# Kernel optimization log

Hardware: AMD Instinct MI355X
Metric: run time of the kernel (lower is better)

Reference implementation:

```python
import jax, jax.numpy as jnp
import numpy as np

N = 100000
E = 1600000
D_IN = 128
HID = 128
OUT = 64


def _sage_conv(x, edge_index, W_l, W_r, b, num_nodes):
    # PyG SAGEConv (aggr='mean'): out = lin_l(mean_{j in N(i)} x_j) + lin_r(x_i)
    src, dst = edge_index[0], edge_index[1]
    msgs = x[src]  # [E, d] gather from source nodes
    summed = jax.ops.segment_sum(msgs, dst, num_segments=num_nodes)  # [N, d]
    cnt = jax.ops.segment_sum(jnp.ones((msgs.shape[0],), x.dtype), dst, num_segments=num_nodes)
    agg = summed / jnp.maximum(cnt, 1.0)[:, None]  # mean; isolated nodes -> 0
    return agg @ W_l + b + x @ W_r


def setup_inputs() -> dict:
    key = jax.random.key(0)
    ks = jax.random.split(key, 8)
    x = jax.random.normal(ks[0], (N, D_IN), dtype=jnp.float32)
    edge_index = jax.random.randint(ks[1], (2, E), 0, N, dtype=jnp.int64)
    s1 = 1.0 / np.sqrt(D_IN)
    s2 = 1.0 / np.sqrt(HID)
    W_l1 = jax.random.uniform(ks[2], (D_IN, HID), jnp.float32, -s1, s1)
    W_r1 = jax.random.uniform(ks[3], (D_IN, HID), jnp.float32, -s1, s1)
    b1 = jnp.zeros((HID,), jnp.float32)
    W_l2 = jax.random.uniform(ks[4], (HID, OUT), jnp.float32, -s2, s2)
    W_r2 = jax.random.uniform(ks[5], (HID, OUT), jnp.float32, -s2, s2)
    b2 = jnp.zeros((OUT,), jnp.float32)
    return {"x": x, "edge_index": edge_index, "W_l1": W_l1, "W_r1": W_r1,
            "b1": b1, "W_l2": W_l2, "W_r2": W_r2, "b2": b2}


def reference(x, edge_index, W_l1, W_r1, b1, W_l2, W_r2, b2):
    h = _sage_conv(x, edge_index, W_l1, W_r1, b1, N)
    h = jax.nn.relu(h)
    out = _sage_conv(h, edge_index, W_l2, W_r2, b2, N)
    return out
```

## Files before the change

kernel.cpp:

```cpp
#include <hip/hip_runtime.h>
#include <hip/hip_fp16.h>

typedef __attribute__((ext_vector_type(8))) short bf16x8;
typedef __attribute__((ext_vector_type(4))) float f32x4;

__device__ __forceinline__ f32x4 mfma16(bf16x8 a, bf16x8 b, f32x4 c) {
    return __builtin_amdgcn_mfma_f32_16x16x32_bf16(a, b, c, 0, 0, 0);
}

__device__ __forceinline__ unsigned short bf16_rte(float f) {
    unsigned int u = __float_as_uint(f);
    unsigned int r = (u + 0x7FFFu + ((u >> 16) & 1u)) >> 16;
    return (unsigned short)r;
}
__device__ __forceinline__ float bf16_f(unsigned short h) {
    return __uint_as_float(((unsigned int)h) << 16);
}

__device__ __forceinline__ void split8h(bf16x8 raw, bf16x8& hi, bf16x8& lo) {
#pragma unroll
    for (int j = 0; j < 8; ++j) {
        float f = __half2float(__ushort_as_half((unsigned short)raw[j]));
        unsigned short h = bf16_rte(f);
        hi[j] = (short)h;
        lo[j] = (short)bf16_rte(f - bf16_f(h));
    }
}

__device__ __forceinline__ void acc8(uint4 r, float4& A0, float4& A1) {
    float2 v0 = __half22float2(*(const __half2*)&r.x);
    float2 v1 = __half22float2(*(const __half2*)&r.y);
    float2 v2 = __half22float2(*(const __half2*)&r.z);
    float2 v3 = __half22float2(*(const __half2*)&r.w);
    A0.x += v0.x; A0.y += v0.y; A0.z += v1.x; A0.w += v1.y;
    A1.x += v2.x; A1.y += v2.y; A1.z += v3.x; A1.w += v3.y;
}

__device__ __forceinline__ void acc4(uint2 r, float4& A) {
    float2 v0 = __half22float2(*(const __half2*)&r.x);
    float2 v1 = __half22float2(*(const __half2*)&r.y);
    A.x += v0.x; A.y += v0.y; A.z += v1.x; A.w += v1.y;
}

#define MAXNB 1024

__global__ __launch_bounds__(256) void k_prep(
    const float* __restrict__ Wl1, const float* __restrict__ Wr1,
    const float* __restrict__ Wl2, const float* __restrict__ Wr2,
    unsigned short* __restrict__ w1ah, unsigned short* __restrict__ w1al,
    unsigned short* __restrict__ w1bh, unsigned short* __restrict__ w1bl,
    unsigned short* __restrict__ w2ah, unsigned short* __restrict__ w2al,
    unsigned short* __restrict__ w2bh, unsigned short* __restrict__ w2bl,
    const float* __restrict__ x, unsigned short* __restrict__ x16,
    const int* __restrict__ dst, int* __restrict__ bcnt,
    int E, int chunk, int xb, int nb, int total8) {
    __shared__ int hh[MAXNB];
    int b = blockIdx.x;
    int t = threadIdx.x;
    if (b < 192) {
        const float* W;
        unsigned short *hi, *lo;
        int F, e;
        if (b < 64)       { W = Wl1; hi = w1ah; lo = w1al; F = 128; e = b * 256 + t; }
        else if (b < 128) { W = Wr1; hi = w1bh; lo = w1bl; F = 128; e = (b - 64) * 256 + t; }
        else if (b < 160) { W = Wl2; hi = w2ah; lo = w2al; F = 64;  e = (b - 128) * 256 + t; }
        else              { W = Wr2; hi = w2bh; lo = w2bl; F = 64;  e = (b - 160) * 256 + t; }
        if (e >= 128 * F) return;
        int col = e >> 7, k = e & 127;
        float v = W[(size_t)k * F + col];
        unsigned short h = bf16_rte(v);
        hi[e] = h;
        lo[e] = bf16_rte(v - bf16_f(h));
    } else if (b < 192 + xb) {
        int i = (b - 192) * 256 + t;
        if (i >= total8) return;
        const float4* xp = (const float4*)x + (size_t)i * 2;
        float4 a = xp[0], bb = xp[1];
        bf16x8 o;
        o[0] = (short)__half_as_ushort(__float2half_rn(a.x));
        o[1] = (short)__half_as_ushort(__float2half_rn(a.y));
        o[2] = (short)__half_as_ushort(__float2half_rn(a.z));
        o[3] = (short)__half_as_ushort(__float2half_rn(a.w));
        o[4] = (short)__half_as_ushort(__float2half_rn(bb.x));
        o[5] = (short)__half_as_ushort(__float2half_rn(bb.y));
        o[6] = (short)__half_as_ushort(__float2half_rn(bb.z));
        o[7] = (short)__half_as_ushort(__float2half_rn(bb.w));
        *(bf16x8*)&x16[(size_t)i * 8] = o;
    } else {
        int cb = b - 192 - xb;
        for (int i = t; i < nb; i += 256) hh[i] = 0;
        __syncthreads();
        int base = cb * chunk;
        int end = min(base + chunk, E);
        for (int i = base + t; i < end; i += 256) atomicAdd(&hh[dst[i] >> 7], 1);
        __syncthreads();
        for (int i = t; i < nb; i += 256)
            if (hh[i]) atomicAdd(&bcnt[i], hh[i]);
    }
}


__global__ void k_bscan(const int* __restrict__ bcnt, int* __restrict__ boff,
                        int* __restrict__ bcur, int nb) {
    __shared__ int sh[1024];
    int t = threadIdx.x;
    int v = (t < nb) ? bcnt[t] : 0;
    sh[t] = v;
    __syncthreads();
    for (int off = 1; off < 1024; off <<= 1) {
        int u = (t >= off) ? sh[t - off] : 0;
        __syncthreads();
        sh[t] += u;
        __syncthreads();
    }
    if (t < nb) {
        int ex = sh[t] - v;
        boff[t] = ex;
        bcur[t] = ex;
    }
}

__global__ __launch_bounds__(256) void k_bscatter(
    const int* __restrict__ src, const int* __restrict__ dst,
    int* __restrict__ bcur, int2* __restrict__ pairs, int E, int chunk, int nb) {
    __shared__ int h[MAXNB];
    __shared__ int curs[MAXNB];
    int t = threadIdx.x;
    for (int i = t; i < nb; i += 256) h[i] = 0;
    __syncthreads();
    int base = blockIdx.x * chunk;
    int end = min(base + chunk, E);
    for (int i = base + t; i < end; i += 256) atomicAdd(&h[dst[i] >> 7], 1);
    __syncthreads();
    for (int i = t; i < nb; i += 256)
        curs[i] = h[i] ? atomicAdd(&bcur[i], h[i]) : 0;
    __syncthreads();
    for (int i = base + t; i < end; i += 256) {
        int d = dst[i];
        int p = atomicAdd(&curs[d >> 7], 1);
        pairs[p] = make_int2(d, src[i]);
    }
}

__global__ __launch_bounds__(256) void k_build(
    const int2* __restrict__ pairs, const int* __restrict__ boff,
    int* __restrict__ csr, int* __restrict__ start, int* __restrict__ deg,
    int n, int nb, int E) {
    __shared__ int scnt[128];
    __shared__ int soff[128];
    __shared__ int cur[128];
    int b = blockIdx.x;
    int t = threadIdx.x;
    int base = boff[b];
    int end = (b + 1 < nb) ? boff[b + 1] : E;
    if (t < 128) scnt[t] = 0;
    __syncthreads();
    for (int i = base + t; i < end; i += 256) {
        int2 e = pairs[i];
        atomicAdd(&scnt[e.x & 127], 1);
    }
    __syncthreads();
    if (t < 128) soff[t] = scnt[t];
    __syncthreads();
    for (int off = 1; off < 128; off <<= 1) {
        int val = 0;
        if (t < 128 && t >= off) val = soff[t - off];
        __syncthreads();
        if (t < 128) soff[t] += val;
        __syncthreads();
    }
    if (t < 128) {
        int c = scnt[t];
        int ex = soff[t] - c;
        int node = b * 128 + t;
        if (node < n) {
            start[node] = base + ex;
            deg[node] = c;
        }
        cur[t] = base + ex;
    }
    __syncthreads();
    for (int i = base + t; i < end; i += 256) {
        int2 e = pairs[i];
        int p = atomicAdd(&cur[e.x & 127], 1);
        csr[p] = e.y;
    }
}

#define SR 40

__global__ __launch_bounds__(256, 2) void fused1(
    const unsigned short* __restrict__ X,
    const int* __restrict__ csr, const int* __restrict__ start,
    const int* __restrict__ deg,
    const unsigned short* __restrict__ W0H, const unsigned short* __restrict__ W0L,
    const unsigned short* __restrict__ W1H, const unsigned short* __restrict__ W1L,
    const float* __restrict__ bias, unsigned short* __restrict__ dstH, int n) {
    constexpr int CT = 2;
    __shared__ unsigned short aHi[4][64 * SR], aLo[4][64 * SR];

    int t = threadIdx.x;
    int wv = t >> 6, l = t & 63, q = l >> 4, nl = l & 15;
    int wc = wv * 32;
    int node0 = blockIdx.x * 64;
    int sn = t >> 2, q4 = t & 3;
    int gn = min(node0 + sn, n - 1);

    {
        const unsigned short* p = X + (size_t)gn * 128 + q4 * 8;
        bf16x8 r[4];
#pragma unroll
        for (int c = 0; c < 4; ++c) r[c] = *(const bf16x8*)(p + c * 32);
        int base = sn * SR + q4 * 8;
#pragma unroll
        for (int c = 0; c < 4; ++c) {
            bf16x8 hi, lo;
            split8h(r[c], hi, lo);
            *(bf16x8*)&aHi[c][base] = hi;
            *(bf16x8*)&aLo[c][base] = lo;
        }
    }

    f32x4 acc[4][CT];
#pragma unroll
    for (int a = 0; a < 4; ++a)
#pragma unroll
        for (int b = 0; b < CT; ++b) acc[a][b] = (f32x4){0.f, 0.f, 0.f, 0.f};

    bf16x8 wh[2][CT], wl[2][CT];
#pragma unroll
    for (int uu = 0; uu < CT; ++uu) {
        int base = (wc + uu * 16 + nl) * 128 + q * 8;
        wh[0][uu] = *(const bf16x8*)&W0H[base];
        wl[0][uu] = *(const bf16x8*)&W0L[base];
    }
    __syncthreads();

#pragma unroll
    for (int c = 0; c < 4; ++c) {
        if (c < 3) {
#pragma unroll
            for (int uu = 0; uu < CT; ++uu) {
                int base = (wc + uu * 16 + nl) * 128 + (c + 1) * 32 + q * 8;
                wh[(c + 1) & 1][uu] = *(const bf16x8*)&W0H[base];
                wl[(c + 1) & 1][uu] = *(const bf16x8*)&W0L[base];
            }
        }
        bf16x8 ah[4], al[4];
#pragma unroll
        for (int tt = 0; tt < 4; ++tt) {
            int off = (tt * 16 + nl) * SR + q * 8;
            ah[tt] = *(const bf16x8*)&aHi[c][off];
            al[tt] = *(const bf16x8*)&aLo[c][off];
        }
        int cb = c & 1;
#pragma unroll
        for (int tt = 0; tt < 4; ++tt)
#pragma unroll
            for (int uu = 0; uu < CT; ++uu) {
                f32x4 a = acc[tt][uu];
                a = mfma16(al[tt], wh[cb][uu], a);
                a = mfma16(ah[tt], wl[cb][uu], a);
                a = mfma16(ah[tt], wh[cb][uu], a);
                acc[tt][uu] = a;
            }
    }
    __syncthreads();

    {
        int sub = l >> 4, fl = l & 15;
        int cch = fl >> 2, qq = fl & 3;
#pragma unroll 1
        for (int r4 = 0; r4 < 4; ++r4) {
            int nloc = wv * 16 + r4 * 4 + sub;
            int nc = min(node0 + nloc, n - 1);
            int s = start[nc], d = deg[nc];
            float4 A0 = {0.f, 0.f, 0.f, 0.f}, A1 = {0.f, 0.f, 0.f, 0.f};
            int j = 0;
            if (d >= 8) {
                int idx[8];
#pragma unroll
                for (int k = 0; k < 8; ++k) idx[k] = csr[s + k];
                for (; j + 16 <= d; j += 8) {
                    uint4 rr[8];
#pragma unroll
                    for (int k = 0; k < 8; ++k)
                        rr[k] = ((const uint4*)(X + (size_t)idx[k] * 128))[fl];
#pragma unroll
                    for (int k = 0; k < 8; ++k) idx[k] = csr[s + j + 8 + k];
#pragma unroll
                    for (int k = 0; k < 8; ++k) acc8(rr[k], A0, A1);
                }
                {
                    uint4 rr[8];
#pragma unroll
                    for (int k = 0; k < 8; ++k)
                        rr[k] = ((const uint4*)(X + (size_t)idx[k] * 128))[fl];
#pragma unroll
                    for (int k = 0; k < 8; ++k) acc8(rr[k], A0, A1);
                    j += 8;
                }
            }
            for (; j < d; ++j)
                acc8(((const uint4*)(X + (size_t)csr[s + j] * 128))[fl], A0, A1);
            float inv = 1.0f / (float)max(d, 1);
            float m[8] = {A0.x * inv, A0.y * inv, A0.z * inv, A0.w * inv,
                          A1.x * inv, A1.y * inv, A1.z * inv, A1.w * inv};
            bf16x8 hi, lo;
#pragma unroll
            for (int k = 0; k < 8; ++k) {
                unsigned short hh = bf16_rte(m[k]);
                hi[k] = (short)hh;
                lo[k] = (short)bf16_rte(m[k] - bf16_f(hh));
            }
            int base = nloc * SR + qq * 8;
            *(bf16x8*)&aHi[cch][base] = hi;
            *(bf16x8*)&aLo[cch][base] = lo;
        }
    }

#pragma unroll
    for (int uu = 0; uu < CT; ++uu) {
        int base = (wc + uu * 16 + nl) * 128 + q * 8;
        wh[0][uu] = *(const bf16x8*)&W1H[base];
        wl[0][uu] = *(const bf16x8*)&W1L[base];
    }
    __syncthreads();

#pragma unroll
    for (int c = 0; c < 4; ++c) {
        if (c < 3) {
#pragma unroll
            for (int uu = 0; uu < CT; ++uu) {
                int base = (wc + uu * 16 + nl) * 128 + (c + 1) * 32 + q * 8;
                wh[(c + 1) & 1][uu] = *(const bf16x8*)&W1H[base];
                wl[(c + 1) & 1][uu] = *(const bf16x8*)&W1L[base];
            }
        }
        bf16x8 ah[4], al[4];
#pragma unroll
        for (int tt = 0; tt < 4; ++tt) {
            int off = (tt * 16 + nl) * SR + q * 8;
            ah[tt] = *(const bf16x8*)&aHi[c][off];
            al[tt] = *(const bf16x8*)&aLo[c][off];
        }
        int cb = c & 1;
#pragma unroll
        for (int tt = 0; tt < 4; ++tt)
#pragma unroll
            for (int uu = 0; uu < CT; ++uu) {
                f32x4 a = acc[tt][uu];
                a = mfma16(al[tt], wh[cb][uu], a);
                a = mfma16(ah[tt], wl[cb][uu], a);
                a = mfma16(ah[tt], wh[cb][uu], a);
                acc[tt][uu] = a;
            }
    }
    __syncthreads();

    unsigned short* tb = &aHi[0][0];
#pragma unroll
    for (int uu = 0; uu < CT; ++uu) {
        int col = wc + uu * 16 + nl;
        float bv = bias[col];
#pragma unroll
        for (int tt = 0; tt < 4; ++tt)
#pragma unroll
            for (int r = 0; r < 4; ++r) {
                float vv = fmaxf(acc[tt][uu][r] + bv, 0.f);
                tb[(tt * 16 + q * 4 + r) * 136 + col] =
                    __half_as_ushort(__float2half_rn(vv));
            }
    }
    __syncthreads();
    int node = node0 + sn;
    if (node < n) {
        const unsigned short* sp = tb + sn * 136 + q4 * 32;
        unsigned short* dp = dstH + (size_t)node * 128 + q4 * 32;
#pragma unroll
        for (int i = 0; i < 4; ++i) *(bf16x8*)(dp + i * 8) = *(const bf16x8*)(sp + i * 8);
    }
}

__global__ __launch_bounds__(256, 2) void gemm2d(
    const unsigned short* __restrict__ H,
    const unsigned short* __restrict__ WaH, const unsigned short* __restrict__ WaL,
    const unsigned short* __restrict__ WbH, const unsigned short* __restrict__ WbL,
    const float* __restrict__ bias, unsigned short* __restrict__ p16,
    float* __restrict__ outF, int n) {
    constexpr int CT = 2;
    __shared__ unsigned short aHi[4][64 * SR], aLo[4][64 * SR];

    int t = threadIdx.x;
    int wv = t >> 6, l = t & 63, q = l >> 4, nl = l & 15;
    int ysel = wv >> 1;
    int wc = (wv & 1) * 32;
    int node0 = blockIdx.x * 64;
    int sn = t >> 2, q4 = t & 3;
    int gn = min(node0 + sn, n - 1);
    const unsigned short* WH = ysel ? WbH : WaH;
    const unsigned short* WL = ysel ? WbL : WaL;

    {
        const unsigned short* p = H + (size_t)gn * 128 + q4 * 8;
        bf16x8 r[4];
#pragma unroll
        for (int c = 0; c < 4; ++c) r[c] = *(const bf16x8*)(p + c * 32);
        int base = sn * SR + q4 * 8;
#pragma unroll
        for (int c = 0; c < 4; ++c) {
            bf16x8 hi, lo;
            split8h(r[c], hi, lo);
            *(bf16x8*)&aHi[c][base] = hi;
            *(bf16x8*)&aLo[c][base] = lo;
        }
    }

    f32x4 acc[4][CT];
#pragma unroll
    for (int a = 0; a < 4; ++a)
#pragma unroll
        for (int b = 0; b < CT; ++b) acc[a][b] = (f32x4){0.f, 0.f, 0.f, 0.f};

    bf16x8 wh[2][CT], wl[2][CT];
#pragma unroll
    for (int uu = 0; uu < CT; ++uu) {
        int base = (wc + uu * 16 + nl) * 128 + q * 8;
        wh[0][uu] = *(const bf16x8*)&WH[base];
        wl[0][uu] = *(const bf16x8*)&WL[base];
    }
    __syncthreads();

#pragma unroll
    for (int c = 0; c < 4; ++c) {
        if (c < 3) {
#pragma unroll
            for (int uu = 0; uu < CT; ++uu) {
                int base = (wc + uu * 16 + nl) * 128 + (c + 1) * 32 + q * 8;
                wh[(c + 1) & 1][uu] = *(const bf16x8*)&WH[base];
                wl[(c + 1) & 1][uu] = *(const bf16x8*)&WL[base];
            }
        }
        bf16x8 ah[4], al[4];
#pragma unroll
        for (int tt = 0; tt < 4; ++tt) {
            int off = (tt * 16 + nl) * SR + q * 8;
            ah[tt] = *(const bf16x8*)&aHi[c][off];
            al[tt] = *(const bf16x8*)&aLo[c][off];
        }
        int cb = c & 1;
#pragma unroll
        for (int tt = 0; tt < 4; ++tt)
#pragma unroll
            for (int uu = 0; uu < CT; ++uu) {
                f32x4 a = acc[tt][uu];
                a = mfma16(al[tt], wh[cb][uu], a);
                a = mfma16(ah[tt], wl[cb][uu], a);
                a = mfma16(ah[tt], wh[cb][uu], a);
                acc[tt][uu] = a;
            }
    }
    __syncthreads();

    unsigned short* tbu = &aHi[0][0];
    float* tbf = (float*)&aLo[0][0];
#pragma unroll
    for (int uu = 0; uu < CT; ++uu) {
        int col = wc + uu * 16 + nl;
        if (ysel) {
            float bv = bias[col];
#pragma unroll
            for (int tt = 0; tt < 4; ++tt)
#pragma unroll
                for (int r = 0; r < 4; ++r)
                    tbf[(tt * 16 + q * 4 + r) * 68 + col] = acc[tt][uu][r] + bv;
        } else {
#pragma unroll
            for (int tt = 0; tt < 4; ++tt)
#pragma unroll
                for (int r = 0; r < 4; ++r)
                    tbu[(tt * 16 + q * 4 + r) * 72 + col] =
                        __half_as_ushort(__float2half_rn(acc[tt][uu][r]));
        }
    }
    __syncthreads();
    int node = node0 + sn;
    if (node < n) {
        const unsigned short* spu = tbu + sn * 72 + q4 * 16;
        unsigned short* dpu = p16 + (size_t)node * 64 + q4 * 16;
        *(bf16x8*)dpu = *(const bf16x8*)spu;
        *(bf16x8*)(dpu + 8) = *(const bf16x8*)(spu + 8);
        const float* spf = tbf + sn * 68 + q4 * 16;
        float* dpf = outF + (size_t)node * 64 + q4 * 16;
#pragma unroll
        for (int i = 0; i < 4; ++i) *(float4*)(dpf + i * 4) = *(const float4*)(spf + i * 4);
    }
}

__global__ __launch_bounds__(256) void aggP(
    const unsigned short* __restrict__ tab, const int* __restrict__ csr,
    const int* __restrict__ start, const int* __restrict__ deg,
    float* __restrict__ outF, int n) {
    int gid = blockIdx.x * blockDim.x + threadIdx.x;
    int wave = gid >> 6, lane = gid & 63;
    int sub = lane >> 4, fl = lane & 15;
    int node = wave * 4 + sub;
    if (node >= n) return;
    int s = start[node], d = deg[node];
    float4 A = {0.f, 0.f, 0.f, 0.f};
    int j = 0;
    if (d >= 8) {
        int idx[8];
#pragma unroll
        for (int k = 0; k < 8; ++k) idx[k] = csr[s + k];
        for (; j + 16 <= d; j += 8) {
            uint2 rr[8];
#pragma unroll
            for (int k = 0; k < 8; ++k)
                rr[k] = ((const uint2*)(tab + (size_t)idx[k] * 64))[fl];
#pragma unroll
            for (int k = 0; k < 8; ++k) idx[k] = csr[s + j + 8 + k];
#pragma unroll
            for (int k = 0; k < 8; ++k) acc4(rr[k], A);
        }
        {
            uint2 rr[8];
#pragma unroll
            for (int k = 0; k < 8; ++k)
                rr[k] = ((const uint2*)(tab + (size_t)idx[k] * 64))[fl];
#pragma unroll
            for (int k = 0; k < 8; ++k) acc4(rr[k], A);
            j += 8;
        }
    }
    for (; j < d; ++j)
        acc4(((const uint2*)(tab + (size_t)csr[s + j] * 64))[fl], A);
    float inv = 1.0f / (float)max(d, 1);
    float* op = outF + (size_t)node * 64 + fl * 4;
    float4 cur = *(float4*)op;
    cur.x += A.x * inv;
    cur.y += A.y * inv;
    cur.z += A.z * inv;
    cur.w += A.w * inv;
    *(float4*)op = cur;
}


extern "C" void kernel_launch(void* const* d_in, const int* in_sizes, int n_in,
                              void* d_out, int out_size, void* d_ws, size_t ws_size,
                              hipStream_t stream) {
    const float* x   = (const float*)d_in[0];
    const int*   ei  = (const int*)d_in[1];
    const float* Wl1 = (const float*)d_in[2];
    const float* Wr1 = (const float*)d_in[3];
    const float* b1  = (const float*)d_in[4];
    const float* Wl2 = (const float*)d_in[5];
    const float* Wr2 = (const float*)d_in[6];
    const float* b2  = (const float*)d_in[7];
    float* out = (float*)d_out;

    int Nn = in_sizes[0] / 128;
    int E  = in_sizes[1] / 2;
    const int* src = ei;
    const int* dst = ei + E;
    int nb = (Nn + 127) / 128;

    char* ws = (char*)d_ws;
    auto alloc = [&](size_t bytes) -> char* {
        char* pp = ws;
        ws += (bytes + 255) / 256 * 256;
        return pp;
    };
    int* bcnt   = (int*)alloc((size_t)nb * 4);
    int* boff   = (int*)alloc((size_t)nb * 4);
    int* bcur   = (int*)alloc((size_t)nb * 4);
    int* start  = (int*)alloc((size_t)Nn * 4);
    int* deg    = (int*)alloc((size_t)Nn * 4);
    int* csr    = (int*)alloc((size_t)E * 4);
    unsigned short* x16  = (unsigned short*)alloc((size_t)Nn * 128 * 2);
    unsigned short* h16  = (unsigned short*)alloc((size_t)Nn * 128 * 2);
    unsigned short* p16  = (unsigned short*)alloc((size_t)Nn * 64 * 2);
    unsigned short* w1ah = (unsigned short*)alloc(128 * 128 * 2);
    unsigned short* w1al = (unsigned short*)alloc(128 * 128 * 2);
    unsigned short* w1bh = (unsigned short*)alloc(128 * 128 * 2);
    unsigned short* w1bl = (unsigned short*)alloc(128 * 128 * 2);
    unsigned short* w2ah = (unsigned short*)alloc(64 * 128 * 2);
    unsigned short* w2al = (unsigned short*)alloc(64 * 128 * 2);
    unsigned short* w2bh = (unsigned short*)alloc(64 * 128 * 2);
    unsigned short* w2bl = (unsigned short*)alloc(64 * 128 * 2);
    int2* pairs = (int2*)p16;

    hipMemsetAsync(bcnt, 0, (size_t)nb * 4, stream);

    int total8 = Nn * 16;
    int xb = (total8 + 255) / 256;
    int chunk = (E + 255) / 256;
    k_prep<<<192 + xb + 256, 256, 0, stream>>>(
        Wl1, Wr1, Wl2, Wr2,
        w1ah, w1al, w1bh, w1bl, w2ah, w2al, w2bh, w2bl,
        x, x16, dst, bcnt, E, chunk, xb, nb, total8);

    k_bscan<<<1, 1024, 0, stream>>>(bcnt, boff, bcur, nb);
    k_bscatter<<<256, 256, 0, stream>>>(src, dst, bcur, pairs, E, chunk, nb);
    k_build<<<nb, 256, 0, stream>>>(pairs, boff, csr, start, deg, Nn, nb, E);

    int gb = (Nn + 63) / 64;
    int ga = (Nn + 15) / 16;
    fused1<<<gb, 256, 0, stream>>>(x16, csr, start, deg,
                                   w1bh, w1bl, w1ah, w1al, b1, h16, Nn);
    gemm2d<<<gb, 256, 0, stream>>>(h16, w2ah, w2al, w2bh, w2bl, b2, p16, out, Nn);
    aggP<<<ga, 256, 0, stream>>>(p16, csr, start, deg, out, Nn);
}
```

Before: 336.1 us.

## Split layer-1 aggregation into standalone kernel and fuse both layer GEMMs

Measured after the change: 328.1 us. -2.4%, faster.

```diff
diff --git a/kernel.cpp b/kernel.cpp
--- a/kernel.cpp
+++ b/kernel.cpp
@@ -189,13 +189,65 @@
 
 #define SR 40
 
-__global__ __launch_bounds__(256, 2) void fused1(
-    const unsigned short* __restrict__ X,
-    const int* __restrict__ csr, const int* __restrict__ start,
-    const int* __restrict__ deg,
+__global__ __launch_bounds__(256) void aggF(
+    const unsigned short* __restrict__ tab, const int* __restrict__ csr,
+    const int* __restrict__ start, const int* __restrict__ deg,
+    unsigned short* __restrict__ outm, int n) {
+    int gid = blockIdx.x * blockDim.x + threadIdx.x;
+    int wave = gid >> 6, lane = gid & 63;
+    int sub = lane >> 4, fl = lane & 15;
+    int node = wave * 4 + sub;
+    if (node >= n) return;
+    int s = start[node], d = deg[node];
+    float4 A0 = {0.f, 0.f, 0.f, 0.f}, A1 = {0.f, 0.f, 0.f, 0.f};
+    int j = 0;
+    if (d >= 4) {
+        int i0 = csr[s], i1 = csr[s + 1], i2 = csr[s + 2], i3 = csr[s + 3];
+        for (; j + 8 <= d; j += 4) {
+            int n0 = csr[s + j + 4], n1 = csr[s + j + 5];
+            int n2 = csr[s + j + 6], n3 = csr[s + j + 7];
+            uint4 r0 = ((const uint4*)(tab + (size_t)i0 * 128))[fl];
+            uint4 r1 = ((const uint4*)(tab + (size_t)i1 * 128))[fl];
+            uint4 r2 = ((const uint4*)(tab + (size_t)i2 * 128))[fl];
+            uint4 r3 = ((const uint4*)(tab + (size_t)i3 * 128))[fl];
+            acc8(r0, A0, A1); acc8(r1, A0, A1);
+            acc8(r2, A0, A1); acc8(r3, A0, A1);
+            i0 = n0; i1 = n1; i2 = n2; i3 = n3;
+        }
+        {
+            uint4 r0 = ((const uint4*)(tab + (size_t)i0 * 128))[fl];
+            uint4 r1 = ((const uint4*)(tab + (size_t)i1 * 128))[fl];
+            uint4 r2 = ((const uint4*)(tab + (size_t)i2 * 128))[fl];
+            uint4 r3 = ((const uint4*)(tab + (size_t)i3 * 128))[fl];
+            acc8(r0, A0, A1); acc8(r1, A0, A1);
+            acc8(r2, A0, A1); acc8(r3, A0, A1);
+            j += 4;
+        }
+    }
+    for (; j < d; ++j)
+        acc8(((const uint4*)(tab + (size_t)csr[s + j] * 128))[fl], A0, A1);
+    float inv = 1.0f / (float)max(d, 1);
+    __half2 h0 = __floats2half2_rn(A0.x * inv, A0.y * inv);
+    __half2 h1 = __floats2half2_rn(A0.z * inv, A0.w * inv);
+    __half2 h2 = __floats2half2_rn(A1.x * inv, A1.y * inv);
+    __half2 h3 = __floats2half2_rn(A1.z * inv, A1.w * inv);
+    uint4 w;
+    w.x = *(unsigned int*)&h0;
+    w.y = *(unsigned int*)&h1;
+    w.z = *(unsigned int*)&h2;
+    w.w = *(unsigned int*)&h3;
+    *(uint4*)&outm[(size_t)node * 128 + fl * 8] = w;
+}
+
+__global__ __launch_bounds__(256, 2) void fused12(
+    const unsigned short* __restrict__ X, const unsigned short* __restrict__ XM,
     const unsigned short* __restrict__ W0H, const unsigned short* __restrict__ W0L,
     const unsigned short* __restrict__ W1H, const unsigned short* __restrict__ W1L,
-    const float* __restrict__ bias, unsigned short* __restrict__ dstH, int n) {
+    const float* __restrict__ b1,
+    const unsigned short* __restrict__ W2aH, const unsigned short* __restrict__ W2aL,
+    const unsigned short* __restrict__ W2bH, const unsigned short* __restrict__ W2bL,
+    const float* __restrict__ b2,
+    unsigned short* __restrict__ p16, float* __restrict__ outF, int n) {
     constexpr int CT = 2;
     __shared__ unsigned short aHi[4][64 * SR], aLo[4][64 * SR];
 
@@ -205,6 +257,20 @@
     int node0 = blockIdx.x * 64;
     int sn = t >> 2, q4 = t & 3;
     int gn = min(node0 + sn, n - 1);
+
+    bf16x8 s1r[4];
+    {
+        const unsigned short* p = XM + (size_t)gn * 128 + q4 * 8;
+#pragma unroll
+        for (int c = 0; c < 4; ++c) s1r[c] = *(const bf16x8*)(p + c * 32);
+    }
+    bf16x8 w1h0[CT], w1l0[CT];
+#pragma unroll
+    for (int uu = 0; uu < CT; ++uu) {
+        int base = (wc + uu * 16 + nl) * 128 + q * 8;
+        w1h0[uu] = *(const bf16x8*)&W1H[base];
+        w1l0[uu] = *(const bf16x8*)&W1L[base];
+    }
 
     {
         const unsigned short* p = X + (size_t)gn * 128 + q4 * 8;
@@ -268,63 +334,17 @@
     __syncthreads();
 
     {
-        int sub = l >> 4, fl = l & 15;
-        int cch = fl >> 2, qq = fl & 3;
-#pragma unroll 1
-        for (int r4 = 0; r4 < 4; ++r4) {
-            int nloc = wv * 16 + r4 * 4 + sub;
-            int nc = min(node0 + nloc, n - 1);
-            int s = start[nc], d = deg[nc];
-            float4 A0 = {0.f, 0.f, 0.f, 0.f}, A1 = {0.f, 0.f, 0.f, 0.f};
-            int j = 0;
-            if (d >= 8) {
-                int idx[8];
-#pragma unroll
-                for (int k = 0; k < 8; ++k) idx[k] = csr[s + k];
-                for (; j + 16 <= d; j += 8) {
-                    uint4 rr[8];
-#pragma unroll
-                    for (int k = 0; k < 8; ++k)
-                        rr[k] = ((const uint4*)(X + (size_t)idx[k] * 128))[fl];
-#pragma unroll
-                    for (int k = 0; k < 8; ++k) idx[k] = csr[s + j + 8 + k];
-#pragma unroll
-                    for (int k = 0; k < 8; ++k) acc8(rr[k], A0, A1);
-                }
-                {
-                    uint4 rr[8];
-#pragma unroll
-                    for (int k = 0; k < 8; ++k)
-                        rr[k] = ((const uint4*)(X + (size_t)idx[k] * 128))[fl];
-#pragma unroll
-                    for (int k = 0; k < 8; ++k) acc8(rr[k], A0, A1);
-                    j += 8;
-                }
-            }
-            for (; j < d; ++j)
-                acc8(((const uint4*)(X + (size_t)csr[s + j] * 128))[fl], A0, A1);
-            float inv = 1.0f / (float)max(d, 1);
-            float m[8] = {A0.x * inv, A0.y * inv, A0.z * inv, A0.w * inv,
-                          A1.x * inv, A1.y * inv, A1.z * inv, A1.w * inv};
+        int base = sn * SR + q4 * 8;
+#pragma unroll
+        for (int c = 0; c < 4; ++c) {
             bf16x8 hi, lo;
-#pragma unroll
-            for (int k = 0; k < 8; ++k) {
-                unsigned short hh = bf16_rte(m[k]);
-                hi[k] = (short)hh;
-                lo[k] = (short)bf16_rte(m[k] - bf16_f(hh));
-            }
-            int base = nloc * SR + qq * 8;
-            *(bf16x8*)&aHi[cch][base] = hi;
-            *(bf16x8*)&aLo[cch][base] = lo;
-        }
-    }
-
-#pragma unroll
-    for (int uu = 0; uu < CT; ++uu) {
-        int base = (wc + uu * 16 + nl) * 128 + q * 8;
-        wh[0][uu] = *(const bf16x8*)&W1H[base];
-        wl[0][uu] = *(const bf16x8*)&W1L[base];
-    }
+            split8h(s1r[c], hi, lo);
+            *(bf16x8*)&aHi[c][base] = hi;
+            *(bf16x8*)&aLo[c][base] = lo;
+        }
+    }
+#pragma unroll
+    for (int uu = 0; uu < CT; ++uu) { wh[0][uu] = w1h0[uu]; wl[0][uu] = w1l0[uu]; }
     __syncthreads();
 
 #pragma unroll
@@ -362,7 +382,7 @@
 #pragma unroll
     for (int uu = 0; uu < CT; ++uu) {
         int col = wc + uu * 16 + nl;
-        float bv = bias[col];
+        float bv = b1[col];
 #pragma unroll
         for (int tt = 0; tt < 4; ++tt)
 #pragma unroll
@@ -373,62 +393,39 @@
             }
     }
     __syncthreads();
-    int node = node0 + sn;
-    if (node < n) {
-        const unsigned short* sp = tb + sn * 136 + q4 * 32;
-        unsigned short* dp = dstH + (size_t)node * 128 + q4 * 32;
-#pragma unroll
-        for (int i = 0; i < 4; ++i) *(bf16x8*)(dp + i * 8) = *(const bf16x8*)(sp + i * 8);
-    }
-}
-
-__global__ __launch_bounds__(256, 2) void gemm2d(
-    const unsigned short* __restrict__ H,
-    const unsigned short* __restrict__ WaH, const unsigned short* __restrict__ WaL,
-    const unsigned short* __restrict__ WbH, const unsigned short* __restrict__ WbL,
-    const float* __restrict__ bias, unsigned short* __restrict__ p16,
-    float* __restrict__ outF, int n) {
-    constexpr int CT = 2;
-    __shared__ unsigned short aHi[4][64 * SR], aLo[4][64 * SR];
-
-    int t = threadIdx.x;
-    int wv = t >> 6, l = t & 63, q = l >> 4, nl = l & 15;
-    int ysel = wv >> 1;
-    int wc = (wv & 1) * 32;
-    int node0 = blockIdx.x * 64;
-    int sn = t >> 2, q4 = t & 3;
-    int gn = min(node0 + sn, n - 1);
-    const unsigned short* WH = ysel ? WbH : WaH;
-    const unsigned short* WL = ysel ? WbL : WaL;
-
+
+    bf16x8 hreg[4];
     {
-        const unsigned short* p = H + (size_t)gn * 128 + q4 * 8;
-        bf16x8 r[4];
-#pragma unroll
-        for (int c = 0; c < 4; ++c) r[c] = *(const bf16x8*)(p + c * 32);
+        const unsigned short* sp = tb + sn * 136 + q4 * 8;
+#pragma unroll
+        for (int c = 0; c < 4; ++c) hreg[c] = *(const bf16x8*)(sp + c * 32);
+    }
+    __syncthreads();
+
+    {
         int base = sn * SR + q4 * 8;
 #pragma unroll
         for (int c = 0; c < 4; ++c) {
             bf16x8 hi, lo;
-            split8h(r[c], hi, lo);
+            split8h(hreg[c], hi, lo);
             *(bf16x8*)&aHi[c][base] = hi;
             *(bf16x8*)&aLo[c][base] = lo;
         }
     }
-
-    f32x4 acc[4][CT];
+    int ysel = wv >> 1;
+    int wc2 = (wv & 1) * 32;
+    const unsigned short* W2H = ysel ? W2bH : W2aH;
+    const unsigned short* W2L = ysel ? W2bL : W2aL;
+#pragma unroll
+    for (int uu = 0; uu < CT; ++uu) {
+        int base = (wc2 + uu * 16 + nl) * 128 + q * 8;
+        wh[0][uu] = *(const bf16x8*)&W2H[base];
+        wl[0][uu] = *(const bf16x8*)&W2L[base];
+    }
 #pragma unroll
     for (int a = 0; a < 4; ++a)
 #pragma unroll
         for (int b = 0; b < CT; ++b) acc[a][b] = (f32x4){0.f, 0.f, 0.f, 0.f};
-
-    bf16x8 wh[2][CT], wl[2][CT];
-#pragma unroll
-    for (int uu = 0; uu < CT; ++uu) {
-        int base = (wc + uu * 16 + nl) * 128 + q * 8;
-        wh[0][uu] = *(const bf16x8*)&WH[base];
-        wl[0][uu] = *(const bf16x8*)&WL[base];
-    }
     __syncthreads();
 
 #pragma unroll
@@ -436,9 +433,9 @@
         if (c < 3) {
 #pragma unroll
             for (int uu = 0; uu < CT; ++uu) {
-                int base = (wc + uu * 16 + nl) * 128 + (c + 1) * 32 + q * 8;
-                wh[(c + 1) & 1][uu] = *(const bf16x8*)&WH[base];
-                wl[(c + 1) & 1][uu] = *(const bf16x8*)&WL[base];
+                int base = (wc2 + uu * 16 + nl) * 128 + (c + 1) * 32 + q * 8;
+                wh[(c + 1) & 1][uu] = *(const bf16x8*)&W2H[base];
+                wl[(c + 1) & 1][uu] = *(const bf16x8*)&W2L[base];
             }
         }
         bf16x8 ah[4], al[4];
@@ -466,9 +463,9 @@
     float* tbf = (float*)&aLo[0][0];
 #pragma unroll
     for (int uu = 0; uu < CT; ++uu) {
-        int col = wc + uu * 16 + nl;
+        int col = wc2 + uu * 16 + nl;
         if (ysel) {
-            float bv = bias[col];
+            float bv = b2[col];
 #pragma unroll
             for (int tt = 0; tt < 4; ++tt)
 #pragma unroll
@@ -578,7 +575,7 @@
     int* deg    = (int*)alloc((size_t)Nn * 4);
     int* csr    = (int*)alloc((size_t)E * 4);
     unsigned short* x16  = (unsigned short*)alloc((size_t)Nn * 128 * 2);
-    unsigned short* h16  = (unsigned short*)alloc((size_t)Nn * 128 * 2);
+    unsigned short* xm16 = (unsigned short*)alloc((size_t)Nn * 128 * 2);
     unsigned short* p16  = (unsigned short*)alloc((size_t)Nn * 64 * 2);
     unsigned short* w1ah = (unsigned short*)alloc(128 * 128 * 2);
     unsigned short* w1al = (unsigned short*)alloc(128 * 128 * 2);
@@ -606,8 +603,10 @@
 
     int gb = (Nn + 63) / 64;
     int ga = (Nn + 15) / 16;
-    fused1<<<gb, 256, 0, stream>>>(x16, csr, start, deg,
-                                   w1bh, w1bl, w1ah, w1al, b1, h16, Nn);
-    gemm2d<<<gb, 256, 0, stream>>>(h16, w2ah, w2al, w2bh, w2bl, b2, p16, out, Nn);
+    aggF<<<ga, 256, 0, stream>>>(x16, csr, start, deg, xm16, Nn);
+    fused12<<<gb, 256, 0, stream>>>(x16, xm16,
+                                    w1bh, w1bl, w1ah, w1al, b1,
+                                    w2ah, w2al, w2bh, w2bl, b2,
+                                    p16, out, Nn);
     aggP<<<ga, 256, 0, stream>>>(p16, csr, start, deg, out, Nn);
 }
```
